# Performance work log

Measured on AMD Instinct MI355X. Metric: run time of the kernel, lower is better.

The kernel has to match this reference:

```python
import jax, jax.numpy as jnp
import numpy as np

B, S, D = 4, 4096, 1024
E = 8            # num_expert_extra + num_expert_proto
F = 2 * D        # ffn_mult * dim
EPS = 1e-5


def setup_inputs() -> dict:
    key = jax.random.key(0)
    ks = jax.random.split(key, 8)
    sc = 0.02
    return {
        "inputs": jax.random.normal(ks[0], (B, S, D), jnp.float32),
        "Wr": jax.random.normal(ks[1], (D, E), jnp.float32) * sc,   # router (no bias)
        "W1": jax.random.normal(ks[2], (E, D, F), jnp.float32) * sc,
        "b1": jnp.zeros((E, F), jnp.float32),
        "gamma": jnp.ones((E, F), jnp.float32),
        "beta": jnp.zeros((E, F), jnp.float32),
        "W2": jax.random.normal(ks[3], (E, F, D), jnp.float32) * sc,
        "b2": jnp.zeros((E, D), jnp.float32),
    }


def reference(inputs, Wr, W1, b1, gamma, beta, W2, b2):
    b, s, d = inputs.shape
    top_k = max(1, int(1.0 * s / E))  # capacity_factor=1.0

    # router: [b, s, e]
    logits = jnp.einsum('bsd,de->bse', inputs, Wr)
    probs = jax.nn.softmax(logits.astype(jnp.float32), axis=-1)

    # expert-choice top-k over tokens: [b, e, k]
    weights, idx = jax.lax.top_k(probs.transpose(0, 2, 1), top_k)

    # gather dispatched tokens: [b, e, k, d]
    bix = jnp.arange(b)[:, None, None]
    xg = inputs[bix, idx]

    # per-expert FFN: fc2(LN(gelu(fc1(x)))) (subln, dropout=eval identity)
    h = jnp.einsum('bekd,edf->bekf', xg, W1) + b1[None, :, None, :]
    h = jax.nn.gelu(h, approximate=False)
    mu = jnp.mean(h, axis=-1, keepdims=True)
    var = jnp.mean(jnp.square(h - mu), axis=-1, keepdims=True)
    h = (h - mu) * jax.lax.rsqrt(var + EPS)
    h = h * gamma[None, :, None, :] + beta[None, :, None, :]
    out = jnp.einsum('bekf,efd->bekd', h, W2) + b2[None, :, None, :]

    # weighted scatter-add back to token positions
    val = weights[..., None].astype(inputs.dtype) * out
    results = jnp.zeros_like(inputs).at[bix, idx].add(val)
    return results, logits
```

## Files before the change

### kernel.cpp

```cpp
#include <hip/hip_runtime.h>
#include <hip/hip_bf16.h>

#define B_ 4
#define S_ 4096
#define D_ 1024
#define E_ 8
#define F_ 2048
#define TK_ 512

typedef unsigned short u16;
typedef unsigned int u32;
typedef u16 u16x4 __attribute__((ext_vector_type(4)));
typedef u16 u16x8 __attribute__((ext_vector_type(8)));
typedef short s16x8 __attribute__((ext_vector_type(8)));
typedef float f32x4 __attribute__((ext_vector_type(4)));

__device__ __forceinline__ u16 f2bf(float f) {
  u32 u = __builtin_bit_cast(u32, f);
  u32 r = (u + 0x7fffu + ((u >> 16) & 1u)) >> 16;
  return (u16)r;
}
__device__ __forceinline__ float b2f(u16 h) {
  return __builtin_bit_cast(float, ((u32)h) << 16);
}
__device__ __forceinline__ void gload16(const u16* g, const u16* l) {
  __builtin_amdgcn_global_load_lds((const __attribute__((address_space(1))) void*)g,
                                   (__attribute__((address_space(3))) void*)l, 16, 0, 0);
}
__device__ __forceinline__ f32x4 mfma_bf16(s16x8 a, s16x8 b, f32x4 c) {
  return __builtin_amdgcn_mfma_f32_16x16x32_bf16(a, b, c, 0, 0, 0);
}

__global__ __launch_bounds__(256) void rc_kernel(const float* __restrict__ x,
                                                 const float* __restrict__ Wr,
                                                 float* __restrict__ logits,
                                                 u16* __restrict__ xb,
                                                 float* __restrict__ results) {
  __shared__ float wr[D_ * E_];
  for (int i = threadIdx.x; i < D_ * E_; i += 256) wr[i] = Wr[i];
  __syncthreads();
  int lane = threadIdx.x & 63;
  int wid = threadIdx.x >> 6;
  int token = blockIdx.x * 4 + wid;
  const float* xr = x + (size_t)token * D_;
  u16* xo = xb + (size_t)token * D_;
  float* ro = results + (size_t)token * D_;
  float acc[E_];
#pragma unroll
  for (int e = 0; e < E_; ++e) acc[e] = 0.f;
#pragma unroll
  for (int q = 0; q < 4; ++q) {
    int d0 = q * 256 + lane * 4;
    float4 v = *(const float4*)(xr + d0);
    u16x4 st;
    st[0] = f2bf(v.x); st[1] = f2bf(v.y); st[2] = f2bf(v.z); st[3] = f2bf(v.w);
    *(u16x4*)(xo + d0) = st;
    *(float4*)(ro + d0) = make_float4(0.f, 0.f, 0.f, 0.f);
    float xv[4] = {v.x, v.y, v.z, v.w};
    const float* w0 = &wr[d0 * E_];
#pragma unroll
    for (int j = 0; j < 4; ++j) {
#pragma unroll
      for (int e = 0; e < E_; ++e) acc[e] += xv[j] * w0[j * E_ + e];
    }
  }
#pragma unroll
  for (int e = 0; e < E_; ++e) {
#pragma unroll
    for (int off = 32; off; off >>= 1) acc[e] += __shfl_down(acc[e], off);
  }
  if (lane == 0) {
    float4 o0 = make_float4(acc[0], acc[1], acc[2], acc[3]);
    float4 o1 = make_float4(acc[4], acc[5], acc[6], acc[7]);
    *(float4*)(logits + (size_t)token * E_) = o0;
    *(float4*)(logits + (size_t)token * E_ + 4) = o1;
  }
}

__device__ __forceinline__ void suffix_scan(u32* h, int n, int tid) {
  for (int d = 1; d < n; d <<= 1) {
    u32 v[2];
    int c = 0;
    for (int i = tid; i < n; i += 1024) v[c++] = (i + d < n) ? h[i + d] : 0;
    __syncthreads();
    c = 0;
    for (int i = tid; i < n; i += 1024) h[i] += v[c++];
    __syncthreads();
  }
}

__global__ __launch_bounds__(1024) void topk_kernel(const float* __restrict__ logits,
                                                    int* __restrict__ idx,
                                                    float* __restrict__ wts) {
  int be = blockIdx.x, b = be >> 3, e = be & 7;
  __shared__ u32 keys[S_];
  __shared__ u32 hist[2048];
  __shared__ u32 tcnt[1024];
  __shared__ u32 sb, sneed, scnt;
  int tid = threadIdx.x;
  const float* lg = logits + (size_t)b * S_ * E_;
  for (int s = tid; s < S_; s += 1024) {
    float4 l0 = *(const float4*)(lg + (size_t)s * E_);
    float4 l1 = *(const float4*)(lg + (size_t)s * E_ + 4);
    float la[8] = {l0.x, l0.y, l0.z, l0.w, l1.x, l1.y, l1.z, l1.w};
    float mx = la[0];
#pragma unroll
    for (int t = 1; t < 8; ++t) mx = fmaxf(mx, la[t]);
    float sum = 0.f;
#pragma unroll
    for (int t = 0; t < 8; ++t) sum += expf(la[t] - mx);
    float p = expf(la[e] - mx) / sum;
    keys[s] = __builtin_bit_cast(u32, p);
  }
  if (tid == 0) scnt = 0;

  hist[tid] = 0; hist[tid + 1024] = 0;
  __syncthreads();
  for (int s = tid; s < S_; s += 1024) atomicAdd(&hist[keys[s] >> 21], 1u);
  __syncthreads();
  suffix_scan(hist, 2048, tid);
  for (int i = tid; i < 2048; i += 1024) {
    u32 nxt = (i + 1 < 2048) ? hist[i + 1] : 0;
    if (hist[i] >= (u32)TK_ && nxt < (u32)TK_) { sb = (u32)i; sneed = TK_ - nxt; }
  }
  __syncthreads();
  u32 b1 = sb, need1 = sneed;
  __syncthreads();

  hist[tid] = 0; hist[tid + 1024] = 0;
  __syncthreads();
  for (int s = tid; s < S_; s += 1024)
    if ((keys[s] >> 21) == b1) atomicAdd(&hist[(keys[s] >> 10) & 2047u], 1u);
  __syncthreads();
  suffix_scan(hist, 2048, tid);
  for (int i = tid; i < 2048; i += 1024) {
    u32 nxt = (i + 1 < 2048) ? hist[i + 1] : 0;
    if (hist[i] >= need1 && nxt < need1) { sb = (u32)i; sneed = need1 - nxt; }
  }
  __syncthreads();
  u32 p2 = (b1 << 11) | sb, need2 = sneed;
  __syncthreads();

  if (tid < 1024) hist[tid] = 0;
  __syncthreads();
  for (int s = tid; s < S_; s += 1024)
    if ((keys[s] >> 10) == p2) atomicAdd(&hist[keys[s] & 1023u], 1u);
  __syncthreads();
  suffix_scan(hist, 1024, tid);
  for (int i = tid; i < 1024; i += 1024) {
    u32 nxt = (i + 1 < 1024) ? hist[i + 1] : 0;
    if (hist[i] >= need2 && nxt < need2) { sb = (u32)i; sneed = need2 - nxt; }
  }
  __syncthreads();
  u32 T = (p2 << 10) | sb;
  u32 needT = sneed;

  for (int s = tid; s < S_; s += 1024) {
    if (keys[s] > T) {
      u32 p = atomicAdd(&scnt, 1u);
      idx[be * TK_ + p] = s;
      wts[be * TK_ + p] = __builtin_bit_cast(float, keys[s]);
    }
  }
  u32 myc = 0;
#pragma unroll
  for (int j = 0; j < 4; ++j) myc += (keys[tid * 4 + j] == T) ? 1u : 0u;
  tcnt[tid] = myc;
  __syncthreads();
  for (int d = 1; d < 1024; d <<= 1) {
    u32 v = (tid >= d) ? tcnt[tid - d] : 0;
    __syncthreads();
    tcnt[tid] += v;
    __syncthreads();
  }
  u32 rank = tcnt[tid] - myc;
#pragma unroll
  for (int j = 0; j < 4; ++j) {
    int s = tid * 4 + j;
    if (keys[s] == T) {
      if (rank < needT) {
        u32 p = atomicAdd(&scnt, 1u);
        idx[be * TK_ + p] = s;
        wts[be * TK_ + p] = __builtin_bit_cast(float, T);
      }
      rank++;
    }
  }
}

__global__ __launch_bounds__(256) void transpose_cvt_kernel(const float* __restrict__ src,
                                                            u16* __restrict__ dst,
                                                            int R, int C,
                                                            const float* __restrict__ scale,
                                                            const float* __restrict__ beta,
                                                            float* __restrict__ Bd) {
  __shared__ float tile[32][33];
  int z = blockIdx.z;
  const float* s = src + (size_t)z * R * C;
  u16* d = dst + (size_t)z * R * C;
  int r0 = blockIdx.x * 32, c0 = blockIdx.y * 32;
  int xx = threadIdx.x & 31, yy = threadIdx.x >> 5;
#pragma unroll
  for (int q = 0; q < 4; ++q)
    tile[yy + q * 8][xx] = s[(size_t)(r0 + yy + q * 8) * C + c0 + xx];
  __syncthreads();
  float sc = scale ? scale[(size_t)z * R + r0 + xx] : 1.f;
#pragma unroll
  for (int q = 0; q < 4; ++q)
    d[(size_t)(c0 + yy + q * 8) * R + r0 + xx] = f2bf(sc * tile[xx][yy + q * 8]);
  if (Bd != nullptr) {
    __syncthreads();
    if (threadIdx.x < 32) {
      float sm = 0.f;
      const float* br = beta + (size_t)z * R + r0;
#pragma unroll
      for (int f = 0; f < 32; ++f) sm += br[f] * tile[f][threadIdx.x];
      unsafeAtomicAdd(&Bd[(size_t)z * C + c0 + threadIdx.x], sm);
    }
  }
}

__global__ __launch_bounds__(256) void gemv_g_kernel(const u16* __restrict__ W2g,
                                                     float* __restrict__ G) {
  int row = blockIdx.x * 4 + (threadIdx.x >> 6);
  int lane = threadIdx.x & 63;
  const u16* wr = W2g + (size_t)row * F_;
  float s = 0.f;
#pragma unroll
  for (int j = 0; j < 4; ++j) {
    u16x8 v = *(const u16x8*)(wr + (j * 64 + lane) * 8);
#pragma unroll
    for (int t = 0; t < 8; ++t) s += b2f(v[t]);
  }
#pragma unroll
  for (int off = 32; off; off >>= 1) s += __shfl_down(s, off);
  if (lane == 0) G[row] = s;
}

__device__ __forceinline__ void kloop97(const u16* const pa[4], const u16* const pb[4],
                                        u16* As, u16* Bs, f32x4 acc[4][4], int NT,
                                        int wid, const int aoff[4], const int boff[4],
                                        int sk0, int sk1) {
  int ldst = wid * 512;
  for (int t = 0; t < NT; ++t) {
    int k0 = t * 64;
#pragma unroll
    for (int q = 0; q < 4; ++q) gload16(pa[q] + k0, As + q * 2048 + ldst);
#pragma unroll
    for (int q = 0; q < 4; ++q) gload16(pb[q] + k0, Bs + q * 2048 + ldst);
    asm volatile("s_waitcnt vmcnt(0)" ::: "memory");
    __builtin_amdgcn_s_barrier();
    s16x8 aF[4], bF[4];
#pragma unroll
    for (int kk = 0; kk < 2; ++kk) {
      int sk = kk ? sk1 : sk0;
#pragma unroll
      for (int f = 0; f < 4; ++f) aF[f] = *(const s16x8*)&As[aoff[f] + sk];
#pragma unroll
      for (int g = 0; g < 4; ++g) bF[g] = *(const s16x8*)&Bs[boff[g] + sk];
      __builtin_amdgcn_s_setprio(1);
#pragma unroll
      for (int f = 0; f < 4; ++f)
#pragma unroll
        for (int g = 0; g < 4; ++g) acc[f][g] = mfma_bf16(aF[f], bF[g], acc[f][g]);
      __builtin_amdgcn_s_setprio(0);
    }
    __builtin_amdgcn_s_barrier();
  }
}

__global__ __launch_bounds__(256, 2) void gemm1_kernel(const u16* __restrict__ xb,
                                                       const u16* __restrict__ W1t,
                                                       const float* __restrict__ b1,
                                                       const int* __restrict__ idx,
                                                       u16* __restrict__ hbuf,
                                                       float2* __restrict__ stats2) {
  int p = blockIdx.x;
  int e = p & 7, slot = p >> 3;
  int tm = slot & 3, bb = (slot >> 2) & 3, tn = slot >> 4;
  int be = bb * 8 + e;
  int t0 = tm * 128, n0 = tn * 128;
  int tid = threadIdx.x, lane = tid & 63, wid = tid >> 6;
  int wm = wid >> 1, wn = wid & 1;
  int cidx = lane & 15, kq = lane >> 4;
  __shared__ u16 As[128 * 64];
  __shared__ u16 Bs[128 * 64];
  __shared__ float2 sm[128][2];

  int srow = tid >> 3;
  int kc = (tid & 7) ^ (srow & 7);
  const u16* pa[4];
  const u16* pb[4];
  const u16* bsrc = W1t + (size_t)e * F_ * D_;
#pragma unroll
  for (int q = 0; q < 4; ++q) {
    int tok = idx[be * TK_ + t0 + q * 32 + srow];
    pa[q] = xb + ((size_t)bb * S_ + tok) * D_ + kc * 8;
    pb[q] = bsrc + (size_t)(n0 + q * 32 + srow) * D_ + kc * 8;
  }
  int aoff[4], boff[4];
#pragma unroll
  for (int f = 0; f < 4; ++f) {
    aoff[f] = (wm * 64 + f * 16 + cidx) * 64;
    boff[f] = (wn * 64 + f * 16 + cidx) * 64;
  }
  int sk0 = (kq ^ (cidx & 7)) * 8;
  int sk1 = ((4 + kq) ^ (cidx & 7)) * 8;

  f32x4 acc[4][4];
#pragma unroll
  for (int f = 0; f < 4; ++f)
#pragma unroll
    for (int g = 0; g < 4; ++g) acc[f][g] = (f32x4){0.f, 0.f, 0.f, 0.f};

  kloop97(pa, pb, As, Bs, acc, D_ / 64, wid, aoff, boff, sk0, sk1);

  float bias[4];
#pragma unroll
  for (int g = 0; g < 4; ++g) bias[g] = b1[e * F_ + n0 + wn * 64 + g * 16 + cidx];
  size_t hbase = (size_t)be * TK_ * F_;
#pragma unroll
  for (int f = 0; f < 4; ++f) {
#pragma unroll
    for (int r = 0; r < 4; ++r) {
      int lr = wm * 64 + f * 16 + kq * 4 + r;
      size_t hb = hbase + (size_t)(t0 + lr) * F_ + n0 + wn * 64 + cidx;
      float vs = 0.f, vss = 0.f;
#pragma unroll
      for (int g = 0; g < 4; ++g) {
        float v = acc[f][g][r] + bias[g];
        float gl = 0.5f * v * (1.0f + erff(v * 0.70710678118654752f));
        hbuf[hb + g * 16] = f2bf(gl);
        vs += gl;
        vss += gl * gl;
      }
#pragma unroll
      for (int off = 1; off < 16; off <<= 1) {
        vs += __shfl_xor(vs, off);
        vss += __shfl_xor(vss, off);
      }
      if (cidx == 0) {
        float2 o; o.x = vs; o.y = vss;
        sm[lr][wn] = o;
      }
    }
  }
  __syncthreads();
  if (tid < 128) {
    float2 a = sm[tid][0], b = sm[tid][1];
    float2 o; o.x = a.x + b.x; o.y = a.y + b.y;
    stats2[((size_t)be * TK_ + t0 + tid) * 16 + tn] = o;
  }
}

__global__ __launch_bounds__(256, 2) void gemm2_kernel(const u16* __restrict__ hbuf,
                                                       const u16* __restrict__ W2g,
                                                       const float* __restrict__ b2,
                                                       const int* __restrict__ idx,
                                                       const float* __restrict__ wts,
                                                       float* __restrict__ results,
                                                       const float2* __restrict__ stats2,
                                                       const float* __restrict__ G,
                                                       const float* __restrict__ Bd) {
  int p = blockIdx.x;
  int e = p & 7, slot = p >> 3;
  int tn = slot & 7, tm = (slot >> 3) & 3, bb = slot >> 5;
  int be = bb * 8 + e;
  int t0 = tm * 128, n0 = tn * 128;
  int tid = threadIdx.x, lane = tid & 63, wid = tid >> 6;
  int wm = wid >> 1, wn = wid & 1;
  int cidx = lane & 15, kq = lane >> 4;
  __shared__ u16 As[128 * 64];
  __shared__ u16 Bs[128 * 64];
  __shared__ float smean[128];
  __shared__ float srstd[128];

  if (tid < 128) {
    const float2* sp = stats2 + ((size_t)be * TK_ + t0 + tid) * 16;
    float sum = 0.f, ss = 0.f;
#pragma unroll
    for (int j = 0; j < 16; ++j) {
      float2 v = sp[j];
      sum += v.x;
      ss += v.y;
    }
    float mean = sum * (1.f / F_);
    float var = ss * (1.f / F_) - mean * mean;
    smean[tid] = mean;
    srstd[tid] = rsqrtf(var + 1e-5f);
  }
  __syncthreads();

  int srow = tid >> 3;
  int kc = (tid & 7) ^ (srow & 7);
  const u16* pa[4];
  const u16* pb[4];
  const u16* asrc = hbuf + (size_t)be * TK_ * F_;
  const u16* bsrc = W2g + (size_t)e * D_ * F_;
#pragma unroll
  for (int q = 0; q < 4; ++q) {
    pa[q] = asrc + (size_t)(t0 + q * 32 + srow) * F_ + kc * 8;
    pb[q] = bsrc + (size_t)(n0 + q * 32 + srow) * F_ + kc * 8;
  }
  int aoff[4], boff[4];
#pragma unroll
  for (int f = 0; f < 4; ++f) {
    aoff[f] = (wm * 64 + f * 16 + cidx) * 64;
    boff[f] = (wn * 64 + f * 16 + cidx) * 64;
  }
  int sk0 = (kq ^ (cidx & 7)) * 8;
  int sk1 = ((4 + kq) ^ (cidx & 7)) * 8;

  f32x4 acc[4][4];
#pragma unroll
  for (int f = 0; f < 4; ++f)
#pragma unroll
    for (int g = 0; g < 4; ++g) acc[f][g] = (f32x4){0.f, 0.f, 0.f, 0.f};

  kloop97(pa, pb, As, Bs, acc, F_ / 64, wid, aoff, boff, sk0, sk1);

  int cb = n0 + wn * 64 + cidx;
  float b2v[4], Gv[4], Bdv[4];
#pragma unroll
  for (int g = 0; g < 4; ++g) {
    b2v[g] = b2[e * D_ + cb + g * 16];
    Gv[g] = G[e * D_ + cb + g * 16];
    Bdv[g] = Bd[e * D_ + cb + g * 16];
  }
#pragma unroll
  for (int f = 0; f < 4; ++f) {
#pragma unroll
    for (int r = 0; r < 4; ++r) {
      int lr = wm * 64 + f * 16 + kq * 4 + r;
      int trow = t0 + lr;
      int tok = idx[be * TK_ + trow];
      float wv = wts[be * TK_ + trow];
      float mean = smean[lr], rstd = srstd[lr];
      float* rrow = results + ((size_t)bb * S_ + tok) * D_ + cb;
#pragma unroll
      for (int g = 0; g < 4; ++g) {
        float out = rstd * acc[f][g][r] - rstd * mean * Gv[g] + Bdv[g] + b2v[g];
        unsafeAtomicAdd(rrow + g * 16, wv * out);
      }
    }
  }
}

extern "C" void kernel_launch(void* const* d_in, const int* in_sizes, int n_in,
                              void* d_out, int out_size, void* d_ws, size_t ws_size,
                              hipStream_t stream) {
  const float* x = (const float*)d_in[0];
  const float* Wr = (const float*)d_in[1];
  const float* W1 = (const float*)d_in[2];
  const float* b1 = (const float*)d_in[3];
  const float* gamma = (const float*)d_in[4];
  const float* beta = (const float*)d_in[5];
  const float* W2 = (const float*)d_in[6];
  const float* b2 = (const float*)d_in[7];

  float* results = (float*)d_out;
  float* logits = results + (size_t)B_ * S_ * D_;

  char* ws = (char*)d_ws;
  const size_t OFF_IDX = 0;
  const size_t OFF_WTS = OFF_IDX + (size_t)B_ * E_ * TK_ * 4;
  const size_t OFF_ST = OFF_WTS + (size_t)B_ * E_ * TK_ * 4;
  const size_t OFF_G = OFF_ST + (size_t)B_ * E_ * TK_ * 16 * 8;
  const size_t OFF_BD = OFF_G + (size_t)E_ * D_ * 4;
  const size_t OFF_R0 = OFF_BD + (size_t)E_ * D_ * 4;
  const size_t OFF_R1 = OFF_R0 + (size_t)E_ * D_ * F_ * 2;
  const size_t OFF_H = OFF_R1 + (size_t)E_ * D_ * F_ * 2;
  const size_t NEED = OFF_H + (size_t)B_ * E_ * TK_ * F_ * 2;
  if (ws_size < NEED) return;

  int* idx = (int*)(ws + OFF_IDX);
  float* wts = (float*)(ws + OFF_WTS);
  float2* stats2 = (float2*)(ws + OFF_ST);
  float* G = (float*)(ws + OFF_G);
  float* Bd = (float*)(ws + OFF_BD);
  u16* xb = (u16*)(ws + OFF_R0);
  u16* W2g = (u16*)(ws + OFF_R0);
  u16* W1t = (u16*)(ws + OFF_R1);
  u16* hbuf = (u16*)(ws + OFF_H);

  rc_kernel<<<dim3(B_ * S_ / 4), 256, 0, stream>>>(x, Wr, logits, xb, results);
  topk_kernel<<<dim3(B_ * E_), 1024, 0, stream>>>(logits, idx, wts);
  transpose_cvt_kernel<<<dim3(D_ / 32, F_ / 32, E_), 256, 0, stream>>>(
      W1, W1t, D_, F_, nullptr, nullptr, nullptr);
  gemm1_kernel<<<dim3(2048), 256, 0, stream>>>(xb, W1t, b1, idx, hbuf, stats2);
  hipMemsetAsync(Bd, 0, (size_t)E_ * D_ * 4, stream);
  transpose_cvt_kernel<<<dim3(F_ / 32, D_ / 32, E_), 256, 0, stream>>>(
      W2, W2g, F_, D_, gamma, beta, Bd);
  gemv_g_kernel<<<dim3(E_ * D_ / 4), 256, 0, stream>>>(W2g, G);
  gemm2_kernel<<<dim3(1024), 256, 0, stream>>>(hbuf, W2g, b2, idx, wts, results,
                                               stats2, G, Bd);
}
```

Baseline: 322.5 us.

## Use 256x256 tiles with 8 waves and double-buffered LDS pipeline in expert GEMMs

Both expert GEMMs move from 128x128 tiles with 4 waves and a single-buffered LDS loop to 256x256 tiles with 8 waves. The K loop now stages the next K-halves into a double buffer while MFMAs run, using partial vmcnt waits and split phases. The goal is more data reuse per LDS load and overlap of global loads with compute. In exchange, the grid shrinks to 512 and 256 blocks, which may underfill the 256 CUs. The larger accumulators also raise register pressure, and LDS use grows to 64KB per block.

```diff
diff --git a/kernel.cpp b/kernel.cpp
--- a/kernel.cpp
+++ b/kernel.cpp
@@ -237,39 +237,61 @@
   if (lane == 0) G[row] = s;
 }
 
-__device__ __forceinline__ void kloop97(const u16* const pa[4], const u16* const pb[4],
-                                        u16* As, u16* Bs, f32x4 acc[4][4], int NT,
-                                        int wid, const int aoff[4], const int boff[4],
-                                        int sk0, int sk1) {
-  int ldst = wid * 512;
-  for (int t = 0; t < NT; ++t) {
-    int k0 = t * 64;
-#pragma unroll
-    for (int q = 0; q < 4; ++q) gload16(pa[q] + k0, As + q * 2048 + ldst);
-#pragma unroll
-    for (int q = 0; q < 4; ++q) gload16(pb[q] + k0, Bs + q * 2048 + ldst);
-    asm volatile("s_waitcnt vmcnt(0)" ::: "memory");
-    __builtin_amdgcn_s_barrier();
-    s16x8 aF[4], bF[4];
-#pragma unroll
-    for (int kk = 0; kk < 2; ++kk) {
-      int sk = kk ? sk1 : sk0;
-#pragma unroll
-      for (int f = 0; f < 4; ++f) aF[f] = *(const s16x8*)&As[aoff[f] + sk];
-#pragma unroll
-      for (int g = 0; g < 4; ++g) bF[g] = *(const s16x8*)&Bs[boff[g] + sk];
-      __builtin_amdgcn_s_setprio(1);
-#pragma unroll
-      for (int f = 0; f < 4; ++f)
-#pragma unroll
-        for (int g = 0; g < 4; ++g) acc[f][g] = mfma_bf16(aF[f], bF[g], acc[f][g]);
-      __builtin_amdgcn_s_setprio(0);
-    }
-    __builtin_amdgcn_s_barrier();
-  }
-}
-
-__global__ __launch_bounds__(256, 2) void gemm1_kernel(const u16* __restrict__ xb,
+#define STG(dst, p0, p1, ko)                                                  \
+  gload16((p0) + (ko), (dst) + tid * 8);                                      \
+  gload16((p1) + (ko), (dst) + 4096 + tid * 8);
+
+#define PHASE(CB, KH, MH, dst, sp0, sp1, ko, DOVM)                            \
+  {                                                                           \
+    s16x8 aF[4];                                                              \
+    _Pragma("unroll") for (int j = 0; j < 4; ++j)                             \
+        aF[j] = *(const s16x8*)&As[CB][KH][aoffs + (MH)*2048 + j * 512];      \
+    if ((MH) == 0) {                                                          \
+      _Pragma("unroll") for (int g = 0; g < 4; ++g)                           \
+          bF[g] = *(const s16x8*)&Bs[CB][KH][boffs + g * 512];                \
+    }                                                                         \
+    STG(dst, sp0, sp1, ko)                                                    \
+    if (DOVM) asm volatile("s_waitcnt vmcnt(4)" ::: "memory");                \
+    __builtin_amdgcn_s_barrier();                                             \
+    __builtin_amdgcn_s_setprio(1);                                            \
+    _Pragma("unroll") for (int j = 0; j < 4; ++j)                             \
+        _Pragma("unroll") for (int g = 0; g < 4; ++g)                         \
+            acc[(MH)*4 + j][g] = mfma_bf16(aF[j], bF[g], acc[(MH)*4 + j][g]); \
+    __builtin_amdgcn_s_setprio(0);                                            \
+    __builtin_amdgcn_s_barrier();                                             \
+  }
+
+#define KTILE8(CB, t)                                                         \
+  {                                                                           \
+    int k1 = ((t) + 1 < NT ? (t) + 1 : 0) * 64;                               \
+    int k2 = ((t) + 2 < NT ? (t) + 2 : 0) * 64;                               \
+    s16x8 bF[4];                                                              \
+    PHASE(CB, 0, 0, &As[(CB) ^ 1][1][0], pa0, pa1, k1 + 32, 0)                \
+    PHASE(CB, 0, 1, &Bs[(CB) ^ 1][1][0], pb0, pb1, k1 + 32, 0)                \
+    PHASE(CB, 1, 0, &As[CB][0][0], pa0, pa1, k2, 0)                           \
+    PHASE(CB, 1, 1, &Bs[CB][0][0], pb0, pb1, k2, 1)                           \
+  }
+
+__device__ __forceinline__ void kloop8(const u16* pa0, const u16* pa1,
+                                       const u16* pb0, const u16* pb1,
+                                       u16 (*As)[2][8192], u16 (*Bs)[2][8192],
+                                       f32x4 acc[8][4], int NT, int tid,
+                                       int aoffs, int boffs) {
+  STG(&As[0][0][0], pa0, pa1, 0)
+  STG(&Bs[0][0][0], pb0, pb1, 0)
+  STG(&As[0][1][0], pa0, pa1, 32)
+  STG(&Bs[0][1][0], pb0, pb1, 32)
+  STG(&As[1][0][0], pa0, pa1, 64)
+  STG(&Bs[1][0][0], pb0, pb1, 64)
+  asm volatile("s_waitcnt vmcnt(4)" ::: "memory");
+  __builtin_amdgcn_s_barrier();
+  for (int t = 0; t < NT; t += 2) {
+    KTILE8(0, t)
+    KTILE8(1, t + 1)
+  }
+}
+
+__global__ __launch_bounds__(512, 2) void gemm1_kernel(const u16* __restrict__ xb,
                                                        const u16* __restrict__ W1t,
                                                        const float* __restrict__ b1,
                                                        const int* __restrict__ idx,
@@ -277,53 +299,47 @@
                                                        float2* __restrict__ stats2) {
   int p = blockIdx.x;
   int e = p & 7, slot = p >> 3;
-  int tm = slot & 3, bb = (slot >> 2) & 3, tn = slot >> 4;
+  int tm = slot & 1, tn = (slot >> 1) & 7, bb = slot >> 4;
   int be = bb * 8 + e;
-  int t0 = tm * 128, n0 = tn * 128;
+  int t0 = tm * 256, n0 = tn * 256;
   int tid = threadIdx.x, lane = tid & 63, wid = tid >> 6;
-  int wm = wid >> 1, wn = wid & 1;
+  int wm = wid >> 2, wn = wid & 3;
   int cidx = lane & 15, kq = lane >> 4;
-  __shared__ u16 As[128 * 64];
-  __shared__ u16 Bs[128 * 64];
-  __shared__ float2 sm[128][2];
-
-  int srow = tid >> 3;
-  int kc = (tid & 7) ^ (srow & 7);
-  const u16* pa[4];
-  const u16* pb[4];
+  __shared__ u16 As[2][2][8192];
+  __shared__ u16 Bs[2][2][8192];
+  __shared__ float2 sm[256][4];
+
+  int srow = tid >> 2;
+  int cc = (tid & 3) ^ ((tid >> 3) & 3);
+  int tokA0 = idx[be * TK_ + t0 + srow];
+  int tokA1 = idx[be * TK_ + t0 + 128 + srow];
   const u16* bsrc = W1t + (size_t)e * F_ * D_;
-#pragma unroll
-  for (int q = 0; q < 4; ++q) {
-    int tok = idx[be * TK_ + t0 + q * 32 + srow];
-    pa[q] = xb + ((size_t)bb * S_ + tok) * D_ + kc * 8;
-    pb[q] = bsrc + (size_t)(n0 + q * 32 + srow) * D_ + kc * 8;
-  }
-  int aoff[4], boff[4];
-#pragma unroll
-  for (int f = 0; f < 4; ++f) {
-    aoff[f] = (wm * 64 + f * 16 + cidx) * 64;
-    boff[f] = (wn * 64 + f * 16 + cidx) * 64;
-  }
-  int sk0 = (kq ^ (cidx & 7)) * 8;
-  int sk1 = ((4 + kq) ^ (cidx & 7)) * 8;
-
-  f32x4 acc[4][4];
-#pragma unroll
-  for (int f = 0; f < 4; ++f)
+  const u16* pa0 = xb + ((size_t)bb * S_ + tokA0) * D_ + cc * 8;
+  const u16* pa1 = xb + ((size_t)bb * S_ + tokA1) * D_ + cc * 8;
+  const u16* pb0 = bsrc + (size_t)(n0 + srow) * D_ + cc * 8;
+  const u16* pb1 = bsrc + (size_t)(n0 + 128 + srow) * D_ + cc * 8;
+
+  int sw8 = (kq ^ ((cidx >> 1) & 3)) * 8;
+  int aoffs = (wm * 128 + cidx) * 32 + sw8;
+  int boffs = (wn * 64 + cidx) * 32 + sw8;
+
+  f32x4 acc[8][4];
+#pragma unroll
+  for (int f = 0; f < 8; ++f)
 #pragma unroll
     for (int g = 0; g < 4; ++g) acc[f][g] = (f32x4){0.f, 0.f, 0.f, 0.f};
 
-  kloop97(pa, pb, As, Bs, acc, D_ / 64, wid, aoff, boff, sk0, sk1);
+  kloop8(pa0, pa1, pb0, pb1, As, Bs, acc, D_ / 64, tid, aoffs, boffs);
 
   float bias[4];
 #pragma unroll
   for (int g = 0; g < 4; ++g) bias[g] = b1[e * F_ + n0 + wn * 64 + g * 16 + cidx];
   size_t hbase = (size_t)be * TK_ * F_;
 #pragma unroll
-  for (int f = 0; f < 4; ++f) {
+  for (int f = 0; f < 8; ++f) {
 #pragma unroll
     for (int r = 0; r < 4; ++r) {
-      int lr = wm * 64 + f * 16 + kq * 4 + r;
+      int lr = wm * 128 + f * 16 + kq * 4 + r;
       size_t hb = hbase + (size_t)(t0 + lr) * F_ + n0 + wn * 64 + cidx;
       float vs = 0.f, vss = 0.f;
 #pragma unroll
@@ -346,14 +362,14 @@
     }
   }
   __syncthreads();
-  if (tid < 128) {
-    float2 a = sm[tid][0], b = sm[tid][1];
-    float2 o; o.x = a.x + b.x; o.y = a.y + b.y;
-    stats2[((size_t)be * TK_ + t0 + tid) * 16 + tn] = o;
-  }
-}
-
-__global__ __launch_bounds__(256, 2) void gemm2_kernel(const u16* __restrict__ hbuf,
+  if (tid < 256) {
+    float2 a0 = sm[tid][0], a1 = sm[tid][1], a2 = sm[tid][2], a3 = sm[tid][3];
+    float2 o; o.x = a0.x + a1.x + a2.x + a3.x; o.y = a0.y + a1.y + a2.y + a3.y;
+    stats2[((size_t)be * TK_ + t0 + tid) * 8 + tn] = o;
+  }
+}
+
+__global__ __launch_bounds__(512, 2) void gemm2_kernel(const u16* __restrict__ hbuf,
                                                        const u16* __restrict__ W2g,
                                                        const float* __restrict__ b2,
                                                        const int* __restrict__ idx,
@@ -364,22 +380,22 @@
                                                        const float* __restrict__ Bd) {
   int p = blockIdx.x;
   int e = p & 7, slot = p >> 3;
-  int tn = slot & 7, tm = (slot >> 3) & 3, bb = slot >> 5;
+  int tn = slot & 3, tm = (slot >> 2) & 1, bb = slot >> 3;
   int be = bb * 8 + e;
-  int t0 = tm * 128, n0 = tn * 128;
+  int t0 = tm * 256, n0 = tn * 256;
   int tid = threadIdx.x, lane = tid & 63, wid = tid >> 6;
-  int wm = wid >> 1, wn = wid & 1;
+  int wm = wid >> 2, wn = wid & 3;
   int cidx = lane & 15, kq = lane >> 4;
-  __shared__ u16 As[128 * 64];
-  __shared__ u16 Bs[128 * 64];
-  __shared__ float smean[128];
-  __shared__ float srstd[128];
-
-  if (tid < 128) {
-    const float2* sp = stats2 + ((size_t)be * TK_ + t0 + tid) * 16;
+  __shared__ u16 As[2][2][8192];
+  __shared__ u16 Bs[2][2][8192];
+  __shared__ float smean[256];
+  __shared__ float srstd[256];
+
+  if (tid < 256) {
+    const float2* sp = stats2 + ((size_t)be * TK_ + t0 + tid) * 8;
     float sum = 0.f, ss = 0.f;
 #pragma unroll
-    for (int j = 0; j < 16; ++j) {
+    for (int j = 0; j < 8; ++j) {
       float2 v = sp[j];
       sum += v.x;
       ss += v.y;
@@ -391,33 +407,26 @@
   }
   __syncthreads();
 
-  int srow = tid >> 3;
-  int kc = (tid & 7) ^ (srow & 7);
-  const u16* pa[4];
-  const u16* pb[4];
+  int srow = tid >> 2;
+  int cc = (tid & 3) ^ ((tid >> 3) & 3);
   const u16* asrc = hbuf + (size_t)be * TK_ * F_;
   const u16* bsrc = W2g + (size_t)e * D_ * F_;
-#pragma unroll
-  for (int q = 0; q < 4; ++q) {
-    pa[q] = asrc + (size_t)(t0 + q * 32 + srow) * F_ + kc * 8;
-    pb[q] = bsrc + (size_t)(n0 + q * 32 + srow) * F_ + kc * 8;
-  }
-  int aoff[4], boff[4];
-#pragma unroll
-  for (int f = 0; f < 4; ++f) {
-    aoff[f] = (wm * 64 + f * 16 + cidx) * 64;
-    boff[f] = (wn * 64 + f * 16 + cidx) * 64;
-  }
-  int sk0 = (kq ^ (cidx & 7)) * 8;
-  int sk1 = ((4 + kq) ^ (cidx & 7)) * 8;
-
-  f32x4 acc[4][4];
-#pragma unroll
-  for (int f = 0; f < 4; ++f)
+  const u16* pa0 = asrc + (size_t)(t0 + srow) * F_ + cc * 8;
+  const u16* pa1 = asrc + (size_t)(t0 + 128 + srow) * F_ + cc * 8;
+  const u16* pb0 = bsrc + (size_t)(n0 + srow) * F_ + cc * 8;
+  const u16* pb1 = bsrc + (size_t)(n0 + 128 + srow) * F_ + cc * 8;
+
+  int sw8 = (kq ^ ((cidx >> 1) & 3)) * 8;
+  int aoffs = (wm * 128 + cidx) * 32 + sw8;
+  int boffs = (wn * 64 + cidx) * 32 + sw8;
+
+  f32x4 acc[8][4];
+#pragma unroll
+  for (int f = 0; f < 8; ++f)
 #pragma unroll
     for (int g = 0; g < 4; ++g) acc[f][g] = (f32x4){0.f, 0.f, 0.f, 0.f};
 
-  kloop97(pa, pb, As, Bs, acc, F_ / 64, wid, aoff, boff, sk0, sk1);
+  kloop8(pa0, pa1, pb0, pb1, As, Bs, acc, F_ / 64, tid, aoffs, boffs);
 
   int cb = n0 + wn * 64 + cidx;
   float b2v[4], Gv[4], Bdv[4];
@@ -428,10 +437,10 @@
     Bdv[g] = Bd[e * D_ + cb + g * 16];
   }
 #pragma unroll
-  for (int f = 0; f < 4; ++f) {
+  for (int f = 0; f < 8; ++f) {
 #pragma unroll
     for (int r = 0; r < 4; ++r) {
-      int lr = wm * 64 + f * 16 + kq * 4 + r;
+      int lr = wm * 128 + f * 16 + kq * 4 + r;
       int trow = t0 + lr;
       int tok = idx[be * TK_ + trow];
       float wv = wts[be * TK_ + trow];
@@ -465,7 +474,7 @@
   const size_t OFF_IDX = 0;
   const size_t OFF_WTS = OFF_IDX + (size_t)B_ * E_ * TK_ * 4;
   const size_t OFF_ST = OFF_WTS + (size_t)B_ * E_ * TK_ * 4;
-  const size_t OFF_G = OFF_ST + (size_t)B_ * E_ * TK_ * 16 * 8;
+  const size_t OFF_G = OFF_ST + (size_t)B_ * E_ * TK_ * 8 * 8;
   const size_t OFF_BD = OFF_G + (size_t)E_ * D_ * 4;
   const size_t OFF_R0 = OFF_BD + (size_t)E_ * D_ * 4;
   const size_t OFF_R1 = OFF_R0 + (size_t)E_ * D_ * F_ * 2;
@@ -487,11 +496,11 @@
   topk_kernel<<<dim3(B_ * E_), 1024, 0, stream>>>(logits, idx, wts);
   transpose_cvt_kernel<<<dim3(D_ / 32, F_ / 32, E_), 256, 0, stream>>>(
       W1, W1t, D_, F_, nullptr, nullptr, nullptr);
-  gemm1_kernel<<<dim3(2048), 256, 0, stream>>>(xb, W1t, b1, idx, hbuf, stats2);
+  gemm1_kernel<<<dim3(512), 512, 0, stream>>>(xb, W1t, b1, idx, hbuf, stats2);
   hipMemsetAsync(Bd, 0, (size_t)E_ * D_ * 4, stream);
   transpose_cvt_kernel<<<dim3(F_ / 32, D_ / 32, E_), 256, 0, stream>>>(
       W2, W2g, F_, D_, gamma, beta, Bd);
   gemv_g_kernel<<<dim3(E_ * D_ / 4), 256, 0, stream>>>(W2g, G);
-  gemm2_kernel<<<dim3(1024), 256, 0, stream>>>(hbuf, W2g, b2, idx, wts, results,
-                                               stats2, G, Bd);
-}
+  gemm2_kernel<<<dim3(256), 512, 0, stream>>>(hbuf, W2g, b2, idx, wts, results,
+                                              stats2, G, Bd);
+}
```

Measured after the change: 417.2 us. 29.4% more time.
